# Optimization experiments

Hardware: AMD Instinct MI355X
Metric: run time of the kernel (lower is better)

Reference implementation:

```python
import jax, jax.numpy as jnp
import numpy as np

UP = jnp.array([0.0, 1.0, 0.0], dtype=jnp.float32)
LEASH = 15.0


def q_inv(q):
    return jnp.concatenate([-q[..., :3], q[..., 3:]], axis=-1)


def q_mul(q1, q2):
    x1, y1, z1, w1 = q1[..., 0], q1[..., 1], q1[..., 2], q1[..., 3]
    x2, y2, z2, w2 = q2[..., 0], q2[..., 1], q2[..., 2], q2[..., 3]
    return jnp.stack([
        w1 * x2 + x1 * w2 + y1 * z2 - z1 * y2,
        w1 * y2 - x1 * z2 + y1 * w2 + z1 * x2,
        w1 * z2 + x1 * y2 - y1 * x2 + z1 * w2,
        w1 * w2 - x1 * x2 - y1 * y2 - z1 * z2], axis=-1)


def q_rot(q, v):
    qv, qw = q[..., :3], q[..., 3:]
    t = 2.0 * jnp.cross(qv, v)
    return v + qw * t + jnp.cross(qv, t)


def mat_to_quat(R):
    # Batched [E,3,3] -> [E,4] (x,y,z,w), matching the torch branch structure.
    r = lambda i, j: R[:, i, j]
    eps = 1e-12
    tr = r(0, 0) + r(1, 1) + r(2, 2)
    Sa = jnp.sqrt(jnp.maximum(tr + 1.0, eps)) * 2.0
    qa = jnp.stack([(r(2, 1) - r(1, 2)) / Sa, (r(0, 2) - r(2, 0)) / Sa,
                    (r(1, 0) - r(0, 1)) / Sa, 0.25 * Sa], -1)
    Sb = jnp.sqrt(jnp.maximum(1.0 + r(0, 0) - r(1, 1) - r(2, 2), eps)) * 2.0
    qb = jnp.stack([0.25 * Sb, (r(0, 1) + r(1, 0)) / Sb,
                    (r(0, 2) + r(2, 0)) / Sb, (r(2, 1) - r(1, 2)) / Sb], -1)
    Sc = jnp.sqrt(jnp.maximum(1.0 + r(1, 1) - r(0, 0) - r(2, 2), eps)) * 2.0
    qc = jnp.stack([(r(0, 1) + r(1, 0)) / Sc, 0.25 * Sc,
                    (r(1, 2) + r(2, 1)) / Sc, (r(0, 2) - r(2, 0)) / Sc], -1)
    Sd = jnp.sqrt(jnp.maximum(1.0 + r(2, 2) - r(0, 0) - r(1, 1), eps)) * 2.0
    qd = jnp.stack([(r(0, 2) + r(2, 0)) / Sd, (r(1, 2) + r(2, 1)) / Sd,
                    0.25 * Sd, (r(1, 0) - r(0, 1)) / Sd], -1)
    cond_b = ((r(0, 0) > r(1, 1)) & (r(0, 0) > r(2, 2)))[:, None]
    cond_c = (r(1, 1) > r(2, 2))[:, None]
    return jnp.where((tr > 0)[:, None], qa,
                     jnp.where(cond_b, qb, jnp.where(cond_c, qc, qd)))


def sfm_pose_loss(pred_t, pred_q, gt_t, gt_q, batch_counts):
    E = batch_counts.shape[0]
    N = pred_t.shape[0]
    counts = batch_counts.astype(jnp.float32)  # [E]
    seg = jnp.repeat(jnp.arange(E), batch_counts, total_repeat_length=N)  # [N]
    starts = jnp.cumsum(batch_counts) - batch_counts  # first index of each episode
    sseg = lambda x: jax.ops.segment_sum(x, seg, num_segments=E)

    # --- per-episode centering ---
    mu_p = sseg(pred_t) / counts[:, None]
    mu_g = sseg(gt_t) / counts[:, None]
    p_c = pred_t - mu_p[seg]
    g_c = gt_t - mu_g[seg]

    # degenerate episodes: too short or near-zero gt variance (unbiased var)
    g_var = sseg(jnp.sum(g_c ** 2, -1)) / (counts - 1.0)
    deg = (batch_counts < 4) | (g_var < 1e-4)  # [E]

    # --- Umeyama: batched 3x3 SVD of H = p_c^T @ g_c per episode ---
    H = sseg(p_c[:, :, None] * g_c[:, None, :])  # [E,3,3]
    H_safe = jnp.where(deg[:, None, None], jnp.diag(jnp.array([3.0, 2.0, 1.0])), H)
    U, S, Vh = jnp.linalg.svd(H_safe, full_matrices=False)
    V = jnp.swapaxes(Vh, -1, -2)
    R0 = jnp.einsum('eij,ekj->eik', V, U)  # V @ U^T
    sgn = jnp.where(jnp.linalg.det(R0) < 0, -1.0, 1.0)
    V_adj = V * jnp.stack([jnp.ones_like(sgn), jnp.ones_like(sgn), sgn], -1)[:, None, :]
    R = jnp.einsum('eij,ekj->eik', V_adj, U)  # [E,3,3]

    p_rot = jnp.einsum('nij,nj->ni', R[seg], p_c)
    denom = sseg(jnp.sum(p_c ** 2, -1))
    nom = sseg(jnp.sum(p_rot * g_c, -1))
    s = jnp.where(denom > 1e-6,
                  jnp.clip(nom / jnp.maximum(denom, 1e-6), 1e-3, 1e3), 1.0)

    # --- translation loss (per-episode mse, then mean over episodes) ---
    p_al = jnp.where(deg[seg][:, None], p_c, p_rot * s[seg][:, None])
    diff = p_al - g_c
    loss_trans = jnp.mean(sseg(jnp.sum(diff ** 2, -1)) / (counts * 3.0))

    # --- scale loss (only non-degenerate episodes) ---
    loss_scale = jnp.sum(jnp.where(deg, 0.0, jnp.log(jnp.abs(s) + 1e-6) ** 2)) / E

    # --- rotation loss ---
    q_align = mat_to_quat(R)  # [E,4]
    q0_p = pred_q[starts]
    q0_g = gt_q[starts]
    pq_deg = q_mul(q_inv(q0_p)[seg], pred_q)
    gq_deg = q_mul(q_inv(q0_g)[seg], gt_q)
    pq_ume = q_mul(q_align[seg], pred_q)
    dm = deg[seg][:, None]
    pq_al = jnp.where(dm, pq_deg, pq_ume)
    gq_al = jnp.where(dm, gq_deg, gt_q)
    dot = jnp.sum(pq_al * gq_al, -1)
    loss_rot = jnp.mean(sseg(1.0 - dot ** 2) / counts)

    # --- gravity loss ---
    up = jnp.broadcast_to(UP, pred_q.shape[:-1] + (3,))
    pu = q_rot(q_inv(pred_q), up)
    gu = q_rot(q_inv(gt_q), up)
    cos = jnp.sum(pu * gu, -1) / jnp.maximum(
        jnp.linalg.norm(pu, axis=-1) * jnp.linalg.norm(gu, axis=-1), 1e-8)
    loss_grav = jnp.mean(sseg(1.0 - cos) / counts)

    # --- frame0 leash (deadzone on first translation of each episode) ---
    mag = jnp.linalg.norm(pred_t[starts], axis=-1)
    loss_leash = jnp.mean(jnp.maximum(mag - LEASH, 0.0) ** 2)

    return jnp.stack([loss_trans, loss_rot, loss_grav, loss_leash, loss_scale])


def setup_inputs() -> dict:
    rng = np.random.default_rng(0)
    E = 4096
    counts = rng.integers(64, 449, size=E)
    counts[:8] = np.array([2, 3, 3, 2, 3, 2, 3, 3])  # exercise degenerate branch
    N = int(counts.sum())
    key = jax.random.key(0)
    k1, k2, k3, k4 = jax.random.split(key, 4)
    pred_t = jax.random.normal(k1, (N, 3), dtype=jnp.float32) * 5.0
    gt_t = jax.random.normal(k2, (N, 3), dtype=jnp.float32) * 5.0

    def rand_unit_quat(k):
        q = jax.random.normal(k, (N, 4), dtype=jnp.float32)
        return q / jnp.linalg.norm(q, axis=-1, keepdims=True)

    return {
        'pred_t': pred_t,
        'pred_q': rand_unit_quat(k3),
        'gt_t': gt_t,
        'gt_q': rand_unit_quat(k4),
        'batch_counts': jnp.asarray(counts, dtype=jnp.int32),
    }


def reference(pred_t, pred_q, gt_t, gt_q, batch_counts):
    # Returns [loss_trans, loss_rot, loss_grav, loss_leash, loss_scale]
    return sfm_pose_loss(pred_t, pred_q, gt_t, gt_q, batch_counts)
```

## Files before the change

kernel.cpp:

```cpp
#include <hip/hip_runtime.h>
#include <math.h>

__global__ void scan_kernel(const int* __restrict__ counts,
                            int* __restrict__ starts,
                            float* __restrict__ out, int E) {
    __shared__ int lds[1024];
    int tid = threadIdx.x;
    if (tid < 5) out[tid] = 0.0f;
    int base = tid * 4;
    int c0 = (base + 0 < E) ? counts[base + 0] : 0;
    int c1 = (base + 1 < E) ? counts[base + 1] : 0;
    int c2 = (base + 2 < E) ? counts[base + 2] : 0;
    int c3 = (base + 3 < E) ? counts[base + 3] : 0;
    lds[tid] = c0 + c1 + c2 + c3;
    __syncthreads();
    for (int off = 1; off < 1024; off <<= 1) {
        int v = lds[tid];
        int a = (tid >= off) ? lds[tid - off] : 0;
        __syncthreads();
        lds[tid] = v + a;
        __syncthreads();
    }
    int excl = (tid > 0) ? lds[tid - 1] : 0;
    if (base + 0 < E) starts[base + 0] = excl; excl += c0;
    if (base + 1 < E) starts[base + 1] = excl; excl += c1;
    if (base + 2 < E) starts[base + 2] = excl; excl += c2;
    if (base + 3 < E) starts[base + 3] = excl;
}

__device__ __forceinline__ float4 qmul4(float4 a, float4 b) {
    return make_float4(
        a.w*b.x + a.x*b.w + a.y*b.z - a.z*b.y,
        a.w*b.y - a.x*b.z + a.y*b.w + a.z*b.x,
        a.w*b.z + a.x*b.y - a.y*b.x + a.z*b.w,
        a.w*b.w - a.x*b.x - a.y*b.y - a.z*b.z);
}

__device__ __forceinline__ void qinv_rot_up(float4 q, float out[3]) {
    float qx = -q.x, qy = -q.y, qz = -q.z, qw = q.w;
    float tx = -2.f*qz;
    float ty = 0.f;
    float tz = 2.f*qx;
    out[0] = 0.f + qw*tx + (qy*tz - qz*ty);
    out[1] = 1.f + qw*ty + (qz*tx - qx*tz);
    out[2] = 0.f + qw*tz + (qx*ty - qy*tx);
}

__device__ __forceinline__ float wave_sum(float v) {
    v += __shfl_xor(v, 32);
    v += __shfl_xor(v, 16);
    v += __shfl_xor(v, 8);
    v += __shfl_xor(v, 4);
    v += __shfl_xor(v, 2);
    v += __shfl_xor(v, 1);
    return v;
}

#define NS 29
__global__ __launch_bounds__(256) void pass1_kernel(
    const float* __restrict__ pred_t, const float4* __restrict__ pred_q,
    const float* __restrict__ gt_t,   const float4* __restrict__ gt_q,
    const int* __restrict__ counts, const int* __restrict__ starts,
    float* __restrict__ segacc, int E)
{
    int wv = threadIdx.x >> 6;
    int lane = threadIdx.x & 63;
    int e = blockIdx.x * 4 + wv;
    if (e >= E) return;
    int start = starts[e];
    int ci = counts[e];
    bool small_c = (ci < 4);
    float4 q0p = pred_q[start];
    float4 q0g = gt_q[start];
    float4 q0pi = make_float4(-q0p.x, -q0p.y, -q0p.z, q0p.w);
    float4 q0gi = make_float4(-q0g.x, -q0g.y, -q0g.z, q0g.w);

    float acc[NS];
    #pragma unroll
    for (int k = 0; k < NS; ++k) acc[k] = 0.f;

    int iters = (ci + 63) >> 6;
    int i = lane;
    int m = start + min(i, ci - 1);
    float px = pred_t[3*m+0], py = pred_t[3*m+1], pz = pred_t[3*m+2];
    float gx = gt_t[3*m+0],  gy = gt_t[3*m+1],  gz = gt_t[3*m+2];
    float4 pq = pred_q[m];
    float4 gq = gt_q[m];

    for (int j = 0; ; ) {
        float npx = 0.f, npy = 0.f, npz = 0.f, ngx = 0.f, ngy = 0.f, ngz = 0.f;
        float4 npq = make_float4(0.f,0.f,0.f,0.f), ngq = npq;
        bool have_next = (j + 1 < iters);
        if (have_next) {
            int m2 = start + min(i + 64, ci - 1);
            npx = pred_t[3*m2+0]; npy = pred_t[3*m2+1]; npz = pred_t[3*m2+2];
            ngx = gt_t[3*m2+0];  ngy = gt_t[3*m2+1];  ngz = gt_t[3*m2+2];
            npq = pred_q[m2];
            ngq = gt_q[m2];
        }
        if (i < ci) {
            acc[0] += px; acc[1] += py; acc[2] += pz;
            acc[3] += gx; acc[4] += gy; acc[5] += gz;
            acc[6] += px*px + py*py + pz*pz;
            acc[7] += gx*gx + gy*gy + gz*gz;
            acc[8]  += px*gx; acc[9]  += px*gy; acc[10] += px*gz;
            acc[11] += py*gx; acc[12] += py*gy; acc[13] += py*gz;
            acc[14] += pz*gx; acc[15] += pz*gy; acc[16] += pz*gz;

            float mx =  pq.w*gq.x - pq.z*gq.y + pq.y*gq.z - pq.x*gq.w;
            float my =  pq.z*gq.x + pq.w*gq.y - pq.x*gq.z - pq.y*gq.w;
            float mz = -pq.y*gq.x + pq.x*gq.y + pq.w*gq.z - pq.z*gq.w;
            float mw =  pq.x*gq.x + pq.y*gq.y + pq.z*gq.z + pq.w*gq.w;
            acc[17] += mx*mx; acc[18] += mx*my; acc[19] += mx*mz; acc[20] += mx*mw;
            acc[21] += my*my; acc[22] += my*mz; acc[23] += my*mw;
            acc[24] += mz*mz; acc[25] += mz*mw; acc[26] += mw*mw;

            float pu[3], gu[3];
            qinv_rot_up(pq, pu);
            qinv_rot_up(gq, gu);
            float cosv = pu[0]*gu[0] + pu[1]*gu[1] + pu[2]*gu[2];
            acc[27] += 1.f - cosv;

            if (small_c) {
                float4 aa = qmul4(q0pi, pq);
                float4 bb = qmul4(q0gi, gq);
                float dd = aa.x*bb.x + aa.y*bb.y + aa.z*bb.z + aa.w*bb.w;
                acc[28] += 1.f - dd*dd;
            }
        }
        if (!have_next) break;
        px = npx; py = npy; pz = npz;
        gx = ngx; gy = ngy; gz = ngz;
        pq = npq; gq = ngq;
        i += 64; ++j;
    }

    #pragma unroll
    for (int k = 0; k < NS; ++k) acc[k] = wave_sum(acc[k]);

    float outv = 0.f;
    #pragma unroll
    for (int k = 0; k < NS; ++k)
        if (lane == k) outv = acc[k];
    if (lane < NS)
        segacc[(size_t)e*32 + lane] = outv;
}

__device__ void jacobi3f(float A[3][3], float V[3][3]) {
    V[0][0]=1.f; V[0][1]=0.f; V[0][2]=0.f;
    V[1][0]=0.f; V[1][1]=1.f; V[1][2]=0.f;
    V[2][0]=0.f; V[2][1]=0.f; V[2][2]=1.f;
    for (int sweep = 0; sweep < 6; ++sweep) {
        float off = A[0][1]*A[0][1] + A[0][2]*A[0][2] + A[1][2]*A[1][2];
        float dia = A[0][0]*A[0][0] + A[1][1]*A[1][1] + A[2][2]*A[2][2];
        if (off <= 1e-12f * (dia + 1e-30f)) break;
        for (int p = 0; p < 2; ++p) for (int q = p + 1; q < 3; ++q) {
            float apq = A[p][q];
            if (fabsf(apq) < 1e-30f) continue;
            float theta = (A[q][q] - A[p][p]) / (2.0f * apq);
            float t = ((theta >= 0.f) ? 1.f : -1.f) / (fabsf(theta) + sqrtf(theta*theta + 1.f));
            float cc = 1.f / sqrtf(t*t + 1.f);
            float ss = t * cc;
            float app = A[p][p], aqq = A[q][q];
            A[p][p] = app - t * apq;
            A[q][q] = aqq + t * apq;
            A[p][q] = 0.f; A[q][p] = 0.f;
            int r = 3 - p - q;
            float arp = A[r][p], arq = A[r][q];
            A[r][p] = cc*arp - ss*arq; A[p][r] = A[r][p];
            A[r][q] = ss*arp + cc*arq; A[q][r] = A[r][q];
            for (int i = 0; i < 3; ++i) {
                float vip = V[i][p], viq = V[i][q];
                V[i][p] = cc*vip - ss*viq;
                V[i][q] = ss*vip + cc*viq;
            }
        }
    }
}

__device__ void mat2quatf(const float R[3][3], float q[4]) {
    const float eps = 1e-12f;
    float tr = R[0][0] + R[1][1] + R[2][2];
    if (tr > 0.f) {
        float S = sqrtf(fmaxf(tr + 1.f, eps)) * 2.f;
        q[0] = (R[2][1]-R[1][2])/S; q[1] = (R[0][2]-R[2][0])/S;
        q[2] = (R[1][0]-R[0][1])/S; q[3] = 0.25f*S;
    } else if ((R[0][0] > R[1][1]) && (R[0][0] > R[2][2])) {
        float S = sqrtf(fmaxf(1.f + R[0][0] - R[1][1] - R[2][2], eps)) * 2.f;
        q[0] = 0.25f*S; q[1] = (R[0][1]+R[1][0])/S;
        q[2] = (R[0][2]+R[2][0])/S; q[3] = (R[2][1]-R[1][2])/S;
    } else if (R[1][1] > R[2][2]) {
        float S = sqrtf(fmaxf(1.f + R[1][1] - R[0][0] - R[2][2], eps)) * 2.f;
        q[0] = (R[0][1]+R[1][0])/S; q[1] = 0.25f*S;
        q[2] = (R[1][2]+R[2][1])/S; q[3] = (R[0][2]-R[2][0])/S;
    } else {
        float S = sqrtf(fmaxf(1.f + R[2][2] - R[0][0] - R[1][1], eps)) * 2.f;
        q[0] = (R[0][2]+R[2][0])/S; q[1] = (R[1][2]+R[2][1])/S;
        q[2] = 0.25f*S; q[3] = (R[1][0]-R[0][1])/S;
    }
}

__global__ __launch_bounds__(64) void finalize_kernel(
    const float* __restrict__ segacc, const int* __restrict__ counts,
    const int* __restrict__ starts, const float* __restrict__ pred_t,
    const float4* __restrict__ pred_q, const float4* __restrict__ gt_q,
    float* __restrict__ out, int E)
{
    int e = blockIdx.x * 64 + threadIdx.x;
    float v_trans = 0.f, v_rot = 0.f, v_grav = 0.f, v_leash = 0.f, v_scale = 0.f;
    if (e < E) {
        const float* A = segacc + (size_t)e * 32;
        int ci = counts[e];
        int start = starts[e];
        float c = (float)ci;
        float mu_p[3] = { A[0]/c, A[1]/c, A[2]/c };
        float mu_g[3] = { A[3]/c, A[4]/c, A[5]/c };
        float pp_c = A[6] - c*(mu_p[0]*mu_p[0]+mu_p[1]*mu_p[1]+mu_p[2]*mu_p[2]);
        float gg_c = A[7] - c*(mu_g[0]*mu_g[0]+mu_g[1]*mu_g[1]+mu_g[2]*mu_g[2]);
        float H[3][3];
        H[0][0]=A[8] -c*mu_p[0]*mu_g[0]; H[0][1]=A[9] -c*mu_p[0]*mu_g[1]; H[0][2]=A[10]-c*mu_p[0]*mu_g[2];
        H[1][0]=A[11]-c*mu_p[1]*mu_g[0]; H[1][1]=A[12]-c*mu_p[1]*mu_g[1]; H[1][2]=A[13]-c*mu_p[1]*mu_g[2];
        H[2][0]=A[14]-c*mu_p[2]*mu_g[0]; H[2][1]=A[15]-c*mu_p[2]*mu_g[1]; H[2][2]=A[16]-c*mu_p[2]*mu_g[2];
        float g_var = gg_c / (c - 1.0f);
        bool small_c = (ci < 4);
        bool deg = small_c || (g_var < 1e-4f);
        float trans, rot, scale = 0.f;
        if (deg) {
            float s28;
            if (small_c) {
                s28 = A[28];
            } else {
                float4 q0p = pred_q[start];
                float4 q0g = gt_q[start];
                float4 q0pi = make_float4(-q0p.x, -q0p.y, -q0p.z, q0p.w);
                float4 q0gi = make_float4(-q0g.x, -q0g.y, -q0g.z, q0g.w);
                float local = 0.f;
                for (int ii = 0; ii < ci; ++ii) {
                    float4 aa = qmul4(q0pi, pred_q[start + ii]);
                    float4 bb = qmul4(q0gi, gt_q[start + ii]);
                    float dd = aa.x*bb.x + aa.y*bb.y + aa.z*bb.z + aa.w*bb.w;
                    local += 1.f - dd*dd;
                }
                s28 = local;
            }
            float trH = H[0][0] + H[1][1] + H[2][2];
            trans = (pp_c - 2.f*trH + gg_c) / (c * 3.f);
            rot = s28 / c;
        } else {
            float B[3][3], V[3][3];
            for (int i = 0; i < 3; ++i)
                for (int j = 0; j < 3; ++j)
                    B[i][j] = H[0][i]*H[0][j] + H[1][i]*H[1][j] + H[2][i]*H[2][j];
            jacobi3f(B, V);
            float lam[3] = { B[0][0], B[1][1], B[2][2] };
            int idx[3] = {0, 1, 2};
            if (lam[idx[0]] < lam[idx[1]]) { int t = idx[0]; idx[0] = idx[1]; idx[1] = t; }
            if (lam[idx[0]] < lam[idx[2]]) { int t = idx[0]; idx[0] = idx[2]; idx[2] = t; }
            if (lam[idx[1]] < lam[idx[2]]) { int t = idx[1]; idx[1] = idx[2]; idx[2] = t; }
            float v1[3], v2[3], v3[3];
            for (int i = 0; i < 3; ++i) { v1[i] = V[i][idx[0]]; v2[i] = V[i][idx[1]]; v3[i] = V[i][idx[2]]; }
            float detV = v1[0]*(v2[1]*v3[2]-v2[2]*v3[1])
                       - v1[1]*(v2[0]*v3[2]-v2[2]*v3[0])
                       + v1[2]*(v2[0]*v3[1]-v2[1]*v3[0]);
            float sgnV = (detV < 0.f) ? -1.f : 1.f;
            float u1[3], u2[3], u3[3];
            for (int i = 0; i < 3; ++i) u1[i] = H[i][0]*v1[0] + H[i][1]*v1[1] + H[i][2]*v1[2];
            float n1 = fmaxf(sqrtf(u1[0]*u1[0]+u1[1]*u1[1]+u1[2]*u1[2]), 1e-30f);
            for (int i = 0; i < 3; ++i) u1[i] /= n1;
            for (int i = 0; i < 3; ++i) u2[i] = H[i][0]*v2[0] + H[i][1]*v2[1] + H[i][2]*v2[2];
            float d12 = u1[0]*u2[0]+u1[1]*u2[1]+u1[2]*u2[2];
            for (int i = 0; i < 3; ++i) u2[i] -= d12*u1[i];
            float n2 = fmaxf(sqrtf(u2[0]*u2[0]+u2[1]*u2[1]+u2[2]*u2[2]), 1e-30f);
            for (int i = 0; i < 3; ++i) u2[i] /= n2;
            u3[0] = u1[1]*u2[2] - u1[2]*u2[1];
            u3[1] = u1[2]*u2[0] - u1[0]*u2[2];
            u3[2] = u1[0]*u2[1] - u1[1]*u2[0];
            float R[3][3];
            for (int i = 0; i < 3; ++i)
                for (int k = 0; k < 3; ++k)
                    R[i][k] = v1[i]*u1[k] + v2[i]*u2[k] + sgnV*v3[i]*u3[k];
            float nom = 0.f;
            for (int k = 0; k < 3; ++k)
                for (int j = 0; j < 3; ++j)
                    nom += R[k][j] * H[j][k];
            float denom = pp_c;
            float s = 1.f;
            if (denom > 1e-6f) {
                s = nom / fmaxf(denom, 1e-6f);
                s = fminf(fmaxf(s, 1e-3f), 1e3f);
            }
            trans = (s*s*denom - 2.f*s*nom + gg_c) / (c * 3.f);
            float ls = logf(fabsf(s) + 1e-6f);
            scale = ls * ls;
            float q[4];
            mat2quatf(R, q);
            float quad = q[0]*q[0]*A[17] + q[1]*q[1]*A[21] + q[2]*q[2]*A[24] + q[3]*q[3]*A[26]
                + 2.f*(q[0]*q[1]*A[18] + q[0]*q[2]*A[19] + q[0]*q[3]*A[20]
                     + q[1]*q[2]*A[22] + q[1]*q[3]*A[23] + q[2]*q[3]*A[25]);
            rot = (c - quad) / c;
        }
        float grav = A[27] / c;
        float tx = pred_t[3*start+0], ty = pred_t[3*start+1], tz = pred_t[3*start+2];
        float mag = sqrtf(tx*tx + ty*ty + tz*tz);
        float ml = fmaxf(mag - 15.f, 0.f);
        float Ed = (float)E;
        v_trans = trans / Ed;
        v_rot   = rot / Ed;
        v_grav  = grav / Ed;
        v_leash = (ml * ml) / Ed;
        v_scale = scale / Ed;
    }
    float vals[5] = { v_trans, v_rot, v_grav, v_leash, v_scale };
    #pragma unroll
    for (int k = 0; k < 5; ++k) {
        float v = wave_sum(vals[k]);
        if (threadIdx.x == 0) atomicAdd(out + k, v);
    }
}

extern "C" void kernel_launch(void* const* d_in, const int* in_sizes, int n_in,
                              void* d_out, int out_size, void* d_ws, size_t ws_size,
                              hipStream_t stream) {
    const float*  pred_t = (const float*)d_in[0];
    const float4* pred_q = (const float4*)d_in[1];
    const float*  gt_t   = (const float*)d_in[2];
    const float4* gt_q   = (const float4*)d_in[3];
    const int*    counts = (const int*)d_in[4];
    int E = in_sizes[4];

    int* starts = (int*)d_ws;
    size_t off = ((size_t)E * sizeof(int) + 255) & ~(size_t)255;
    float* segacc = (float*)((char*)d_ws + off);

    scan_kernel<<<1, 1024, 0, stream>>>(counts, starts, (float*)d_out, E);
    pass1_kernel<<<(E + 3) / 4, 256, 0, stream>>>(pred_t, pred_q, gt_t, gt_q,
                                                  counts, starts, segacc, E);
    finalize_kernel<<<(E + 63) / 64, 64, 0, stream>>>(segacc, counts, starts, pred_t,
                                                      pred_q, gt_q, (float*)d_out, E);
}
```

Baseline: 118.6 us.

## Fuse per-episode reduction and finalize into one kernel with wave-parallel fallback

Merges the per-episode accumulation kernel and the finalize kernel into a single kernel. Each wave runs the Procrustes/SVD finalize redundantly across its lanes right after its reduction, then issues per-wave atomics into the five outputs. This removes one launch and the segacc round trip through global memory. The degenerate-variance fallback loop also becomes lane-parallel instead of serial per thread. In exchange, the serial Jacobi/SVD math now runs once per wave instead of once per thread, and there are many more atomics on five addresses (4096 waves × 5).

```diff
diff --git a/kernel.cpp b/kernel.cpp
--- a/kernel.cpp
+++ b/kernel.cpp
@@ -54,96 +54,6 @@
     v += __shfl_xor(v, 2);
     v += __shfl_xor(v, 1);
     return v;
-}
-
-#define NS 29
-__global__ __launch_bounds__(256) void pass1_kernel(
-    const float* __restrict__ pred_t, const float4* __restrict__ pred_q,
-    const float* __restrict__ gt_t,   const float4* __restrict__ gt_q,
-    const int* __restrict__ counts, const int* __restrict__ starts,
-    float* __restrict__ segacc, int E)
-{
-    int wv = threadIdx.x >> 6;
-    int lane = threadIdx.x & 63;
-    int e = blockIdx.x * 4 + wv;
-    if (e >= E) return;
-    int start = starts[e];
-    int ci = counts[e];
-    bool small_c = (ci < 4);
-    float4 q0p = pred_q[start];
-    float4 q0g = gt_q[start];
-    float4 q0pi = make_float4(-q0p.x, -q0p.y, -q0p.z, q0p.w);
-    float4 q0gi = make_float4(-q0g.x, -q0g.y, -q0g.z, q0g.w);
-
-    float acc[NS];
-    #pragma unroll
-    for (int k = 0; k < NS; ++k) acc[k] = 0.f;
-
-    int iters = (ci + 63) >> 6;
-    int i = lane;
-    int m = start + min(i, ci - 1);
-    float px = pred_t[3*m+0], py = pred_t[3*m+1], pz = pred_t[3*m+2];
-    float gx = gt_t[3*m+0],  gy = gt_t[3*m+1],  gz = gt_t[3*m+2];
-    float4 pq = pred_q[m];
-    float4 gq = gt_q[m];
-
-    for (int j = 0; ; ) {
-        float npx = 0.f, npy = 0.f, npz = 0.f, ngx = 0.f, ngy = 0.f, ngz = 0.f;
-        float4 npq = make_float4(0.f,0.f,0.f,0.f), ngq = npq;
-        bool have_next = (j + 1 < iters);
-        if (have_next) {
-            int m2 = start + min(i + 64, ci - 1);
-            npx = pred_t[3*m2+0]; npy = pred_t[3*m2+1]; npz = pred_t[3*m2+2];
-            ngx = gt_t[3*m2+0];  ngy = gt_t[3*m2+1];  ngz = gt_t[3*m2+2];
-            npq = pred_q[m2];
-            ngq = gt_q[m2];
-        }
-        if (i < ci) {
-            acc[0] += px; acc[1] += py; acc[2] += pz;
-            acc[3] += gx; acc[4] += gy; acc[5] += gz;
-            acc[6] += px*px + py*py + pz*pz;
-            acc[7] += gx*gx + gy*gy + gz*gz;
-            acc[8]  += px*gx; acc[9]  += px*gy; acc[10] += px*gz;
-            acc[11] += py*gx; acc[12] += py*gy; acc[13] += py*gz;
-            acc[14] += pz*gx; acc[15] += pz*gy; acc[16] += pz*gz;
-
-            float mx =  pq.w*gq.x - pq.z*gq.y + pq.y*gq.z - pq.x*gq.w;
-            float my =  pq.z*gq.x + pq.w*gq.y - pq.x*gq.z - pq.y*gq.w;
-            float mz = -pq.y*gq.x + pq.x*gq.y + pq.w*gq.z - pq.z*gq.w;
-            float mw =  pq.x*gq.x + pq.y*gq.y + pq.z*gq.z + pq.w*gq.w;
-            acc[17] += mx*mx; acc[18] += mx*my; acc[19] += mx*mz; acc[20] += mx*mw;
-            acc[21] += my*my; acc[22] += my*mz; acc[23] += my*mw;
-            acc[24] += mz*mz; acc[25] += mz*mw; acc[26] += mw*mw;
-
-            float pu[3], gu[3];
-            qinv_rot_up(pq, pu);
-            qinv_rot_up(gq, gu);
-            float cosv = pu[0]*gu[0] + pu[1]*gu[1] + pu[2]*gu[2];
-            acc[27] += 1.f - cosv;
-
-            if (small_c) {
-                float4 aa = qmul4(q0pi, pq);
-                float4 bb = qmul4(q0gi, gq);
-                float dd = aa.x*bb.x + aa.y*bb.y + aa.z*bb.z + aa.w*bb.w;
-                acc[28] += 1.f - dd*dd;
-            }
-        }
-        if (!have_next) break;
-        px = npx; py = npy; pz = npz;
-        gx = ngx; gy = ngy; gz = ngz;
-        pq = npq; gq = ngq;
-        i += 64; ++j;
-    }
-
-    #pragma unroll
-    for (int k = 0; k < NS; ++k) acc[k] = wave_sum(acc[k]);
-
-    float outv = 0.f;
-    #pragma unroll
-    for (int k = 0; k < NS; ++k)
-        if (lane == k) outv = acc[k];
-    if (lane < NS)
-        segacc[(size_t)e*32 + lane] = outv;
 }
 
 __device__ void jacobi3f(float A[3][3], float V[3][3]) {
@@ -200,122 +110,188 @@
     }
 }
 
-__global__ __launch_bounds__(64) void finalize_kernel(
-    const float* __restrict__ segacc, const int* __restrict__ counts,
-    const int* __restrict__ starts, const float* __restrict__ pred_t,
-    const float4* __restrict__ pred_q, const float4* __restrict__ gt_q,
+#define NS 29
+__global__ __launch_bounds__(256) void fused_kernel(
+    const float* __restrict__ pred_t, const float4* __restrict__ pred_q,
+    const float* __restrict__ gt_t,   const float4* __restrict__ gt_q,
+    const int* __restrict__ counts, const int* __restrict__ starts,
     float* __restrict__ out, int E)
 {
-    int e = blockIdx.x * 64 + threadIdx.x;
-    float v_trans = 0.f, v_rot = 0.f, v_grav = 0.f, v_leash = 0.f, v_scale = 0.f;
-    if (e < E) {
-        const float* A = segacc + (size_t)e * 32;
-        int ci = counts[e];
-        int start = starts[e];
-        float c = (float)ci;
-        float mu_p[3] = { A[0]/c, A[1]/c, A[2]/c };
-        float mu_g[3] = { A[3]/c, A[4]/c, A[5]/c };
-        float pp_c = A[6] - c*(mu_p[0]*mu_p[0]+mu_p[1]*mu_p[1]+mu_p[2]*mu_p[2]);
-        float gg_c = A[7] - c*(mu_g[0]*mu_g[0]+mu_g[1]*mu_g[1]+mu_g[2]*mu_g[2]);
-        float H[3][3];
-        H[0][0]=A[8] -c*mu_p[0]*mu_g[0]; H[0][1]=A[9] -c*mu_p[0]*mu_g[1]; H[0][2]=A[10]-c*mu_p[0]*mu_g[2];
-        H[1][0]=A[11]-c*mu_p[1]*mu_g[0]; H[1][1]=A[12]-c*mu_p[1]*mu_g[1]; H[1][2]=A[13]-c*mu_p[1]*mu_g[2];
-        H[2][0]=A[14]-c*mu_p[2]*mu_g[0]; H[2][1]=A[15]-c*mu_p[2]*mu_g[1]; H[2][2]=A[16]-c*mu_p[2]*mu_g[2];
-        float g_var = gg_c / (c - 1.0f);
-        bool small_c = (ci < 4);
-        bool deg = small_c || (g_var < 1e-4f);
-        float trans, rot, scale = 0.f;
-        if (deg) {
-            float s28;
+    int wv = threadIdx.x >> 6;
+    int lane = threadIdx.x & 63;
+    int e = blockIdx.x * 4 + wv;
+    if (e >= E) return;
+    int start = starts[e];
+    int ci = counts[e];
+    bool small_c = (ci < 4);
+    float4 q0p = pred_q[start];
+    float4 q0g = gt_q[start];
+    float4 q0pi = make_float4(-q0p.x, -q0p.y, -q0p.z, q0p.w);
+    float4 q0gi = make_float4(-q0g.x, -q0g.y, -q0g.z, q0g.w);
+
+    float acc[NS];
+    #pragma unroll
+    for (int k = 0; k < NS; ++k) acc[k] = 0.f;
+
+    int iters = (ci + 63) >> 6;
+    int i = lane;
+    int m = start + min(i, ci - 1);
+    float px = pred_t[3*m+0], py = pred_t[3*m+1], pz = pred_t[3*m+2];
+    float gx = gt_t[3*m+0],  gy = gt_t[3*m+1],  gz = gt_t[3*m+2];
+    float4 pq = pred_q[m];
+    float4 gq = gt_q[m];
+
+    for (int j = 0; ; ) {
+        float npx = 0.f, npy = 0.f, npz = 0.f, ngx = 0.f, ngy = 0.f, ngz = 0.f;
+        float4 npq = make_float4(0.f,0.f,0.f,0.f), ngq = npq;
+        bool have_next = (j + 1 < iters);
+        if (have_next) {
+            int m2 = start + min(i + 64, ci - 1);
+            npx = pred_t[3*m2+0]; npy = pred_t[3*m2+1]; npz = pred_t[3*m2+2];
+            ngx = gt_t[3*m2+0];  ngy = gt_t[3*m2+1];  ngz = gt_t[3*m2+2];
+            npq = pred_q[m2];
+            ngq = gt_q[m2];
+        }
+        if (i < ci) {
+            acc[0] += px; acc[1] += py; acc[2] += pz;
+            acc[3] += gx; acc[4] += gy; acc[5] += gz;
+            acc[6] += px*px + py*py + pz*pz;
+            acc[7] += gx*gx + gy*gy + gz*gz;
+            acc[8]  += px*gx; acc[9]  += px*gy; acc[10] += px*gz;
+            acc[11] += py*gx; acc[12] += py*gy; acc[13] += py*gz;
+            acc[14] += pz*gx; acc[15] += pz*gy; acc[16] += pz*gz;
+
+            float mx =  pq.w*gq.x - pq.z*gq.y + pq.y*gq.z - pq.x*gq.w;
+            float my =  pq.z*gq.x + pq.w*gq.y - pq.x*gq.z - pq.y*gq.w;
+            float mz = -pq.y*gq.x + pq.x*gq.y + pq.w*gq.z - pq.z*gq.w;
+            float mw =  pq.x*gq.x + pq.y*gq.y + pq.z*gq.z + pq.w*gq.w;
+            acc[17] += mx*mx; acc[18] += mx*my; acc[19] += mx*mz; acc[20] += mx*mw;
+            acc[21] += my*my; acc[22] += my*mz; acc[23] += my*mw;
+            acc[24] += mz*mz; acc[25] += mz*mw; acc[26] += mw*mw;
+
+            float pu[3], gu[3];
+            qinv_rot_up(pq, pu);
+            qinv_rot_up(gq, gu);
+            float cosv = pu[0]*gu[0] + pu[1]*gu[1] + pu[2]*gu[2];
+            acc[27] += 1.f - cosv;
+
             if (small_c) {
-                s28 = A[28];
-            } else {
-                float4 q0p = pred_q[start];
-                float4 q0g = gt_q[start];
-                float4 q0pi = make_float4(-q0p.x, -q0p.y, -q0p.z, q0p.w);
-                float4 q0gi = make_float4(-q0g.x, -q0g.y, -q0g.z, q0g.w);
-                float local = 0.f;
-                for (int ii = 0; ii < ci; ++ii) {
-                    float4 aa = qmul4(q0pi, pred_q[start + ii]);
-                    float4 bb = qmul4(q0gi, gt_q[start + ii]);
-                    float dd = aa.x*bb.x + aa.y*bb.y + aa.z*bb.z + aa.w*bb.w;
-                    local += 1.f - dd*dd;
-                }
-                s28 = local;
+                float4 aa = qmul4(q0pi, pq);
+                float4 bb = qmul4(q0gi, gq);
+                float dd = aa.x*bb.x + aa.y*bb.y + aa.z*bb.z + aa.w*bb.w;
+                acc[28] += 1.f - dd*dd;
             }
-            float trH = H[0][0] + H[1][1] + H[2][2];
-            trans = (pp_c - 2.f*trH + gg_c) / (c * 3.f);
-            rot = s28 / c;
+        }
+        if (!have_next) break;
+        px = npx; py = npy; pz = npz;
+        gx = ngx; gy = ngy; gz = ngz;
+        pq = npq; gq = ngq;
+        i += 64; ++j;
+    }
+
+    #pragma unroll
+    for (int k = 0; k < NS; ++k) acc[k] = wave_sum(acc[k]);
+
+    float c = (float)ci;
+    float mu_p[3] = { acc[0]/c, acc[1]/c, acc[2]/c };
+    float mu_g[3] = { acc[3]/c, acc[4]/c, acc[5]/c };
+    float pp_c = acc[6] - c*(mu_p[0]*mu_p[0]+mu_p[1]*mu_p[1]+mu_p[2]*mu_p[2]);
+    float gg_c = acc[7] - c*(mu_g[0]*mu_g[0]+mu_g[1]*mu_g[1]+mu_g[2]*mu_g[2]);
+    float H[3][3];
+    H[0][0]=acc[8] -c*mu_p[0]*mu_g[0]; H[0][1]=acc[9] -c*mu_p[0]*mu_g[1]; H[0][2]=acc[10]-c*mu_p[0]*mu_g[2];
+    H[1][0]=acc[11]-c*mu_p[1]*mu_g[0]; H[1][1]=acc[12]-c*mu_p[1]*mu_g[1]; H[1][2]=acc[13]-c*mu_p[1]*mu_g[2];
+    H[2][0]=acc[14]-c*mu_p[2]*mu_g[0]; H[2][1]=acc[15]-c*mu_p[2]*mu_g[1]; H[2][2]=acc[16]-c*mu_p[2]*mu_g[2];
+    float g_var = gg_c / (c - 1.0f);
+    bool deg = small_c || (g_var < 1e-4f);
+    float trans, rot, scale = 0.f;
+    if (deg) {
+        float s28;
+        if (small_c) {
+            s28 = acc[28];
         } else {
-            float B[3][3], V[3][3];
-            for (int i = 0; i < 3; ++i)
-                for (int j = 0; j < 3; ++j)
-                    B[i][j] = H[0][i]*H[0][j] + H[1][i]*H[1][j] + H[2][i]*H[2][j];
-            jacobi3f(B, V);
-            float lam[3] = { B[0][0], B[1][1], B[2][2] };
-            int idx[3] = {0, 1, 2};
-            if (lam[idx[0]] < lam[idx[1]]) { int t = idx[0]; idx[0] = idx[1]; idx[1] = t; }
-            if (lam[idx[0]] < lam[idx[2]]) { int t = idx[0]; idx[0] = idx[2]; idx[2] = t; }
-            if (lam[idx[1]] < lam[idx[2]]) { int t = idx[1]; idx[1] = idx[2]; idx[2] = t; }
-            float v1[3], v2[3], v3[3];
-            for (int i = 0; i < 3; ++i) { v1[i] = V[i][idx[0]]; v2[i] = V[i][idx[1]]; v3[i] = V[i][idx[2]]; }
-            float detV = v1[0]*(v2[1]*v3[2]-v2[2]*v3[1])
-                       - v1[1]*(v2[0]*v3[2]-v2[2]*v3[0])
-                       + v1[2]*(v2[0]*v3[1]-v2[1]*v3[0]);
-            float sgnV = (detV < 0.f) ? -1.f : 1.f;
-            float u1[3], u2[3], u3[3];
-            for (int i = 0; i < 3; ++i) u1[i] = H[i][0]*v1[0] + H[i][1]*v1[1] + H[i][2]*v1[2];
-            float n1 = fmaxf(sqrtf(u1[0]*u1[0]+u1[1]*u1[1]+u1[2]*u1[2]), 1e-30f);
-            for (int i = 0; i < 3; ++i) u1[i] /= n1;
-            for (int i = 0; i < 3; ++i) u2[i] = H[i][0]*v2[0] + H[i][1]*v2[1] + H[i][2]*v2[2];
-            float d12 = u1[0]*u2[0]+u1[1]*u2[1]+u1[2]*u2[2];
-            for (int i = 0; i < 3; ++i) u2[i] -= d12*u1[i];
-            float n2 = fmaxf(sqrtf(u2[0]*u2[0]+u2[1]*u2[1]+u2[2]*u2[2]), 1e-30f);
-            for (int i = 0; i < 3; ++i) u2[i] /= n2;
-            u3[0] = u1[1]*u2[2] - u1[2]*u2[1];
-            u3[1] = u1[2]*u2[0] - u1[0]*u2[2];
-            u3[2] = u1[0]*u2[1] - u1[1]*u2[0];
-            float R[3][3];
-            for (int i = 0; i < 3; ++i)
-                for (int k = 0; k < 3; ++k)
-                    R[i][k] = v1[i]*u1[k] + v2[i]*u2[k] + sgnV*v3[i]*u3[k];
-            float nom = 0.f;
-            for (int k = 0; k < 3; ++k)
-                for (int j = 0; j < 3; ++j)
-                    nom += R[k][j] * H[j][k];
-            float denom = pp_c;
-            float s = 1.f;
-            if (denom > 1e-6f) {
-                s = nom / fmaxf(denom, 1e-6f);
-                s = fminf(fmaxf(s, 1e-3f), 1e3f);
+            float local = 0.f;
+            for (int ii = lane; ii < ci; ii += 64) {
+                float4 aa = qmul4(q0pi, pred_q[start + ii]);
+                float4 bb = qmul4(q0gi, gt_q[start + ii]);
+                float dd = aa.x*bb.x + aa.y*bb.y + aa.z*bb.z + aa.w*bb.w;
+                local += 1.f - dd*dd;
             }
-            trans = (s*s*denom - 2.f*s*nom + gg_c) / (c * 3.f);
-            float ls = logf(fabsf(s) + 1e-6f);
-            scale = ls * ls;
-            float q[4];
-            mat2quatf(R, q);
-            float quad = q[0]*q[0]*A[17] + q[1]*q[1]*A[21] + q[2]*q[2]*A[24] + q[3]*q[3]*A[26]
-                + 2.f*(q[0]*q[1]*A[18] + q[0]*q[2]*A[19] + q[0]*q[3]*A[20]
-                     + q[1]*q[2]*A[22] + q[1]*q[3]*A[23] + q[2]*q[3]*A[25]);
-            rot = (c - quad) / c;
-        }
-        float grav = A[27] / c;
-        float tx = pred_t[3*start+0], ty = pred_t[3*start+1], tz = pred_t[3*start+2];
-        float mag = sqrtf(tx*tx + ty*ty + tz*tz);
-        float ml = fmaxf(mag - 15.f, 0.f);
-        float Ed = (float)E;
-        v_trans = trans / Ed;
-        v_rot   = rot / Ed;
-        v_grav  = grav / Ed;
-        v_leash = (ml * ml) / Ed;
-        v_scale = scale / Ed;
-    }
-    float vals[5] = { v_trans, v_rot, v_grav, v_leash, v_scale };
-    #pragma unroll
-    for (int k = 0; k < 5; ++k) {
-        float v = wave_sum(vals[k]);
-        if (threadIdx.x == 0) atomicAdd(out + k, v);
-    }
+            s28 = wave_sum(local);
+        }
+        float trH = H[0][0] + H[1][1] + H[2][2];
+        trans = (pp_c - 2.f*trH + gg_c) / (c * 3.f);
+        rot = s28 / c;
+    } else {
+        float B[3][3], V[3][3];
+        for (int ii = 0; ii < 3; ++ii)
+            for (int jj = 0; jj < 3; ++jj)
+                B[ii][jj] = H[0][ii]*H[0][jj] + H[1][ii]*H[1][jj] + H[2][ii]*H[2][jj];
+        jacobi3f(B, V);
+        float lam[3] = { B[0][0], B[1][1], B[2][2] };
+        int idx[3] = {0, 1, 2};
+        if (lam[idx[0]] < lam[idx[1]]) { int t = idx[0]; idx[0] = idx[1]; idx[1] = t; }
+        if (lam[idx[0]] < lam[idx[2]]) { int t = idx[0]; idx[0] = idx[2]; idx[2] = t; }
+        if (lam[idx[1]] < lam[idx[2]]) { int t = idx[1]; idx[1] = idx[2]; idx[2] = t; }
+        float v1[3], v2[3], v3[3];
+        for (int ii = 0; ii < 3; ++ii) { v1[ii] = V[ii][idx[0]]; v2[ii] = V[ii][idx[1]]; v3[ii] = V[ii][idx[2]]; }
+        float detV = v1[0]*(v2[1]*v3[2]-v2[2]*v3[1])
+                   - v1[1]*(v2[0]*v3[2]-v2[2]*v3[0])
+                   + v1[2]*(v2[0]*v3[1]-v2[1]*v3[0]);
+        float sgnV = (detV < 0.f) ? -1.f : 1.f;
+        float u1[3], u2[3], u3[3];
+        for (int ii = 0; ii < 3; ++ii) u1[ii] = H[ii][0]*v1[0] + H[ii][1]*v1[1] + H[ii][2]*v1[2];
+        float n1 = fmaxf(sqrtf(u1[0]*u1[0]+u1[1]*u1[1]+u1[2]*u1[2]), 1e-30f);
+        for (int ii = 0; ii < 3; ++ii) u1[ii] /= n1;
+        for (int ii = 0; ii < 3; ++ii) u2[ii] = H[ii][0]*v2[0] + H[ii][1]*v2[1] + H[ii][2]*v2[2];
+        float d12 = u1[0]*u2[0]+u1[1]*u2[1]+u1[2]*u2[2];
+        for (int ii = 0; ii < 3; ++ii) u2[ii] -= d12*u1[ii];
+        float n2 = fmaxf(sqrtf(u2[0]*u2[0]+u2[1]*u2[1]+u2[2]*u2[2]), 1e-30f);
+        for (int ii = 0; ii < 3; ++ii) u2[ii] /= n2;
+        u3[0] = u1[1]*u2[2] - u1[2]*u2[1];
+        u3[1] = u1[2]*u2[0] - u1[0]*u2[2];
+        u3[2] = u1[0]*u2[1] - u1[1]*u2[0];
+        float R[3][3];
+        for (int ii = 0; ii < 3; ++ii)
+            for (int kk = 0; kk < 3; ++kk)
+                R[ii][kk] = v1[ii]*u1[kk] + v2[ii]*u2[kk] + sgnV*v3[ii]*u3[kk];
+        float nom = 0.f;
+        for (int kk = 0; kk < 3; ++kk)
+            for (int jj = 0; jj < 3; ++jj)
+                nom += R[kk][jj] * H[jj][kk];
+        float denom = pp_c;
+        float s = 1.f;
+        if (denom > 1e-6f) {
+            s = nom / fmaxf(denom, 1e-6f);
+            s = fminf(fmaxf(s, 1e-3f), 1e3f);
+        }
+        trans = (s*s*denom - 2.f*s*nom + gg_c) / (c * 3.f);
+        float ls = logf(fabsf(s) + 1e-6f);
+        scale = ls * ls;
+        float q[4];
+        mat2quatf(R, q);
+        float quad = q[0]*q[0]*acc[17] + q[1]*q[1]*acc[21] + q[2]*q[2]*acc[24] + q[3]*q[3]*acc[26]
+            + 2.f*(q[0]*q[1]*acc[18] + q[0]*q[2]*acc[19] + q[0]*q[3]*acc[20]
+                 + q[1]*q[2]*acc[22] + q[1]*q[3]*acc[23] + q[2]*q[3]*acc[25]);
+        rot = (c - quad) / c;
+    }
+    float grav = acc[27] / c;
+    float tx = pred_t[3*start+0], ty = pred_t[3*start+1], tz = pred_t[3*start+2];
+    float mag = sqrtf(tx*tx + ty*ty + tz*tz);
+    float ml = fmaxf(mag - 15.f, 0.f);
+    float Ed = (float)E;
+    float v_trans = trans / Ed;
+    float v_rot   = rot / Ed;
+    float v_grav  = grav / Ed;
+    float v_leash = (ml * ml) / Ed;
+    float v_scale = scale / Ed;
+
+    float outv = 0.f;
+    if (lane == 0) outv = v_trans;
+    else if (lane == 1) outv = v_rot;
+    else if (lane == 2) outv = v_grav;
+    else if (lane == 3) outv = v_leash;
+    else if (lane == 4) outv = v_scale;
+    if (lane < 5) atomicAdd(out + lane, outv);
 }
 
 extern "C" void kernel_launch(void* const* d_in, const int* in_sizes, int n_in,
@@ -329,12 +305,8 @@
     int E = in_sizes[4];
 
     int* starts = (int*)d_ws;
-    size_t off = ((size_t)E * sizeof(int) + 255) & ~(size_t)255;
-    float* segacc = (float*)((char*)d_ws + off);
 
     scan_kernel<<<1, 1024, 0, stream>>>(counts, starts, (float*)d_out, E);
-    pass1_kernel<<<(E + 3) / 4, 256, 0, stream>>>(pred_t, pred_q, gt_t, gt_q,
-                                                  counts, starts, segacc, E);
-    finalize_kernel<<<(E + 63) / 64, 64, 0, stream>>>(segacc, counts, starts, pred_t,
-                                                      pred_q, gt_q, (float*)d_out, E);
-}
+    fused_kernel<<<(E + 3) / 4, 256, 0, stream>>>(pred_t, pred_q, gt_t, gt_q,
+                                                  counts, starts, (float*)d_out, E);
+}
```

After: 158.9 us. 34.0% more time.

## Split each episode across chunked grid dimension with partial sums reduced in finalize

Applied to the files above, without the earlier changes.

pass1 now launches a 2D grid where blockIdx.y selects one of four 128-point chunks, so each wave handles only part of an episode instead of the whole thing. Each chunk writes a separate 32-float partial row, and finalize sums the partial rows of every active chunk before it solves. The goal is more parallelism and shorter per-wave serial loops for long episodes. The cost is more workspace traffic, an extra read-and-sum step in finalize, and the loss of the explicit software prefetch the old loop used.

```diff
diff --git a/kernel.cpp b/kernel.cpp
--- a/kernel.cpp
+++ b/kernel.cpp
@@ -57,82 +57,85 @@
 }
 
 #define NS 29
+#define CHUNK 128
+#define NCH 4
+
+__device__ __forceinline__ void accum_point(
+    int i, int ci, int start,
+    const float* __restrict__ pred_t, const float4* __restrict__ pred_q,
+    const float* __restrict__ gt_t,   const float4* __restrict__ gt_q,
+    bool small_c, float4 q0pi, float4 q0gi, float acc[NS])
+{
+    int m = start + min(i, ci - 1);
+    float px = pred_t[3*m+0], py = pred_t[3*m+1], pz = pred_t[3*m+2];
+    float gx = gt_t[3*m+0],  gy = gt_t[3*m+1],  gz = gt_t[3*m+2];
+    float4 pq = pred_q[m];
+    float4 gq = gt_q[m];
+    if (i < ci) {
+        acc[0] += px; acc[1] += py; acc[2] += pz;
+        acc[3] += gx; acc[4] += gy; acc[5] += gz;
+        acc[6] += px*px + py*py + pz*pz;
+        acc[7] += gx*gx + gy*gy + gz*gz;
+        acc[8]  += px*gx; acc[9]  += px*gy; acc[10] += px*gz;
+        acc[11] += py*gx; acc[12] += py*gy; acc[13] += py*gz;
+        acc[14] += pz*gx; acc[15] += pz*gy; acc[16] += pz*gz;
+
+        float mx =  pq.w*gq.x - pq.z*gq.y + pq.y*gq.z - pq.x*gq.w;
+        float my =  pq.z*gq.x + pq.w*gq.y - pq.x*gq.z - pq.y*gq.w;
+        float mz = -pq.y*gq.x + pq.x*gq.y + pq.w*gq.z - pq.z*gq.w;
+        float mw =  pq.x*gq.x + pq.y*gq.y + pq.z*gq.z + pq.w*gq.w;
+        acc[17] += mx*mx; acc[18] += mx*my; acc[19] += mx*mz; acc[20] += mx*mw;
+        acc[21] += my*my; acc[22] += my*mz; acc[23] += my*mw;
+        acc[24] += mz*mz; acc[25] += mz*mw; acc[26] += mw*mw;
+
+        float pu[3], gu[3];
+        qinv_rot_up(pq, pu);
+        qinv_rot_up(gq, gu);
+        float cosv = pu[0]*gu[0] + pu[1]*gu[1] + pu[2]*gu[2];
+        acc[27] += 1.f - cosv;
+
+        if (small_c) {
+            float4 aa = qmul4(q0pi, pq);
+            float4 bb = qmul4(q0gi, gq);
+            float dd = aa.x*bb.x + aa.y*bb.y + aa.z*bb.z + aa.w*bb.w;
+            acc[28] += 1.f - dd*dd;
+        }
+    }
+}
+
 __global__ __launch_bounds__(256) void pass1_kernel(
     const float* __restrict__ pred_t, const float4* __restrict__ pred_q,
     const float* __restrict__ gt_t,   const float4* __restrict__ gt_q,
     const int* __restrict__ counts, const int* __restrict__ starts,
-    float* __restrict__ segacc, int E)
+    float* __restrict__ P, int E)
 {
     int wv = threadIdx.x >> 6;
     int lane = threadIdx.x & 63;
     int e = blockIdx.x * 4 + wv;
     if (e >= E) return;
+    int ci = counts[e];
+    int ch = blockIdx.y;
+    int base0 = ch * CHUNK;
+    if (base0 >= ci) return;
     int start = starts[e];
-    int ci = counts[e];
     bool small_c = (ci < 4);
-    float4 q0p = pred_q[start];
-    float4 q0g = gt_q[start];
-    float4 q0pi = make_float4(-q0p.x, -q0p.y, -q0p.z, q0p.w);
-    float4 q0gi = make_float4(-q0g.x, -q0g.y, -q0g.z, q0g.w);
+    float4 q0pi = make_float4(0.f,0.f,0.f,0.f), q0gi = q0pi;
+    if (small_c) {
+        float4 q0p = pred_q[start];
+        float4 q0g = gt_q[start];
+        q0pi = make_float4(-q0p.x, -q0p.y, -q0p.z, q0p.w);
+        q0gi = make_float4(-q0g.x, -q0g.y, -q0g.z, q0g.w);
+    }
 
     float acc[NS];
     #pragma unroll
     for (int k = 0; k < NS; ++k) acc[k] = 0.f;
 
-    int iters = (ci + 63) >> 6;
-    int i = lane;
-    int m = start + min(i, ci - 1);
-    float px = pred_t[3*m+0], py = pred_t[3*m+1], pz = pred_t[3*m+2];
-    float gx = gt_t[3*m+0],  gy = gt_t[3*m+1],  gz = gt_t[3*m+2];
-    float4 pq = pred_q[m];
-    float4 gq = gt_q[m];
-
-    for (int j = 0; ; ) {
-        float npx = 0.f, npy = 0.f, npz = 0.f, ngx = 0.f, ngy = 0.f, ngz = 0.f;
-        float4 npq = make_float4(0.f,0.f,0.f,0.f), ngq = npq;
-        bool have_next = (j + 1 < iters);
-        if (have_next) {
-            int m2 = start + min(i + 64, ci - 1);
-            npx = pred_t[3*m2+0]; npy = pred_t[3*m2+1]; npz = pred_t[3*m2+2];
-            ngx = gt_t[3*m2+0];  ngy = gt_t[3*m2+1];  ngz = gt_t[3*m2+2];
-            npq = pred_q[m2];
-            ngq = gt_q[m2];
-        }
-        if (i < ci) {
-            acc[0] += px; acc[1] += py; acc[2] += pz;
-            acc[3] += gx; acc[4] += gy; acc[5] += gz;
-            acc[6] += px*px + py*py + pz*pz;
-            acc[7] += gx*gx + gy*gy + gz*gz;
-            acc[8]  += px*gx; acc[9]  += px*gy; acc[10] += px*gz;
-            acc[11] += py*gx; acc[12] += py*gy; acc[13] += py*gz;
-            acc[14] += pz*gx; acc[15] += pz*gy; acc[16] += pz*gz;
-
-            float mx =  pq.w*gq.x - pq.z*gq.y + pq.y*gq.z - pq.x*gq.w;
-            float my =  pq.z*gq.x + pq.w*gq.y - pq.x*gq.z - pq.y*gq.w;
-            float mz = -pq.y*gq.x + pq.x*gq.y + pq.w*gq.z - pq.z*gq.w;
-            float mw =  pq.x*gq.x + pq.y*gq.y + pq.z*gq.z + pq.w*gq.w;
-            acc[17] += mx*mx; acc[18] += mx*my; acc[19] += mx*mz; acc[20] += mx*mw;
-            acc[21] += my*my; acc[22] += my*mz; acc[23] += my*mw;
-            acc[24] += mz*mz; acc[25] += mz*mw; acc[26] += mw*mw;
-
-            float pu[3], gu[3];
-            qinv_rot_up(pq, pu);
-            qinv_rot_up(gq, gu);
-            float cosv = pu[0]*gu[0] + pu[1]*gu[1] + pu[2]*gu[2];
-            acc[27] += 1.f - cosv;
-
-            if (small_c) {
-                float4 aa = qmul4(q0pi, pq);
-                float4 bb = qmul4(q0gi, gq);
-                float dd = aa.x*bb.x + aa.y*bb.y + aa.z*bb.z + aa.w*bb.w;
-                acc[28] += 1.f - dd*dd;
-            }
-        }
-        if (!have_next) break;
-        px = npx; py = npy; pz = npz;
-        gx = ngx; gy = ngy; gz = ngz;
-        pq = npq; gq = ngq;
-        i += 64; ++j;
+    for (int base = base0; base < ci; base += NCH * CHUNK) {
+        accum_point(base + lane,      ci, start, pred_t, pred_q, gt_t, gt_q,
+                    small_c, q0pi, q0gi, acc);
+        accum_point(base + 64 + lane, ci, start, pred_t, pred_q, gt_t, gt_q,
+                    small_c, q0pi, q0gi, acc);
     }
 
     #pragma unroll
@@ -142,8 +145,8 @@
     #pragma unroll
     for (int k = 0; k < NS; ++k)
         if (lane == k) outv = acc[k];
-    if (lane < NS)
-        segacc[(size_t)e*32 + lane] = outv;
+    if (lane < 32)
+        P[((size_t)ch * E + e) * 32 + lane] = outv;
 }
 
 __device__ void jacobi3f(float A[3][3], float V[3][3]) {
@@ -201,7 +204,7 @@
 }
 
 __global__ __launch_bounds__(64) void finalize_kernel(
-    const float* __restrict__ segacc, const int* __restrict__ counts,
+    const float* __restrict__ P, const int* __restrict__ counts,
     const int* __restrict__ starts, const float* __restrict__ pred_t,
     const float4* __restrict__ pred_q, const float4* __restrict__ gt_q,
     float* __restrict__ out, int E)
@@ -209,9 +212,23 @@
     int e = blockIdx.x * 64 + threadIdx.x;
     float v_trans = 0.f, v_rot = 0.f, v_grav = 0.f, v_leash = 0.f, v_scale = 0.f;
     if (e < E) {
-        const float* A = segacc + (size_t)e * 32;
         int ci = counts[e];
         int start = starts[e];
+        float A[32];
+        #pragma unroll
+        for (int k = 0; k < 32; ++k) A[k] = 0.f;
+        #pragma unroll
+        for (int ch = 0; ch < NCH; ++ch) {
+            if (ch * CHUNK < ci) {
+                const float4* rp = (const float4*)(P + ((size_t)ch * E + e) * 32);
+                #pragma unroll
+                for (int j = 0; j < 8; ++j) {
+                    float4 v = rp[j];
+                    A[4*j+0] += v.x; A[4*j+1] += v.y;
+                    A[4*j+2] += v.z; A[4*j+3] += v.w;
+                }
+            }
+        }
         float c = (float)ci;
         float mu_p[3] = { A[0]/c, A[1]/c, A[2]/c };
         float mu_g[3] = { A[3]/c, A[4]/c, A[5]/c };
@@ -330,11 +347,12 @@
 
     int* starts = (int*)d_ws;
     size_t off = ((size_t)E * sizeof(int) + 255) & ~(size_t)255;
-    float* segacc = (float*)((char*)d_ws + off);
+    float* P = (float*)((char*)d_ws + off);
 
     scan_kernel<<<1, 1024, 0, stream>>>(counts, starts, (float*)d_out, E);
-    pass1_kernel<<<(E + 3) / 4, 256, 0, stream>>>(pred_t, pred_q, gt_t, gt_q,
-                                                  counts, starts, segacc, E);
-    finalize_kernel<<<(E + 63) / 64, 64, 0, stream>>>(segacc, counts, starts, pred_t,
+    dim3 g1((E + 3) / 4, NCH);
+    pass1_kernel<<<g1, 256, 0, stream>>>(pred_t, pred_q, gt_t, gt_q,
+                                         counts, starts, P, E);
+    finalize_kernel<<<(E + 63) / 64, 64, 0, stream>>>(P, counts, starts, pred_t,
                                                       pred_q, gt_q, (float*)d_out, E);
 }
```

After: 129.7 us. +9.4%, slower.
